# Optimization experiments

Measured on AMD Instinct MI355X. Metric: run time of the kernel, lower is better.

Reference implementation:

```python
import jax, jax.numpy as jnp
import numpy as np

TRAIN_COUNT, FEAT = 20000, 40
BATCH, NN, M = 2048, 64, 10


def _safe_l2(d2):
    # sqrt with zero (not NaN/inf) gradient at d2 == 0 (diagonal of pairwise dists)
    pos = d2 > 0
    return jnp.where(pos, jnp.sqrt(jnp.where(pos, d2, 1.0)), 0.0)


def setup_inputs() -> dict:
    key = jax.random.key(0)
    k1, k2, k3, k4 = jax.random.split(key, 4)
    x = jax.random.normal(k1, (TRAIN_COUNT, FEAT), dtype=jnp.float32)
    batch_indices = jax.random.randint(k2, (BATCH,), 0, TRAIN_COUNT)
    batch_nn_indices = jax.random.randint(k3, (BATCH, NN), 0, TRAIN_COUNT)
    batch_nn_targets = jax.random.normal(k4, (BATCH, NN, M), dtype=jnp.float32)
    length_scale = jnp.ones((M,), dtype=jnp.float32)
    eps = 1e-3 * jnp.ones((M,), dtype=jnp.float32)
    return {
        "x": x,
        "length_scale": length_scale,
        "eps": eps,
        "batch_indices": batch_indices,
        "batch_nn_indices": batch_nn_indices,
        "batch_nn_targets": batch_nn_targets,
    }


def reference(x, length_scale, eps, batch_indices, batch_nn_indices, batch_nn_targets):
    b, nn, m = batch_nn_targets.shape
    xb = x[batch_indices]          # (b, f)
    xn = x[batch_nn_indices]       # (b, nn, f)

    # crosswise l2 distances (b, nn)
    cd = _safe_l2(jnp.sum((xb[:, None, :] - xn) ** 2, axis=-1))
    # pairwise l2 distances (b, nn, nn)
    pd = _safe_l2(jnp.sum((xn[:, :, None, :] - xn[:, None, :, :]) ** 2, axis=-1))

    # Matern nu = 1/2: k(d) = exp(-d / length_scale); vectorized over the m models
    Kcross = jnp.exp(-cd[None, :, :] / length_scale[:, None, None])            # (m, b, nn)
    K = jnp.exp(-pd[None, :, :, :] / length_scale[:, None, None, None])        # (m, b, nn, nn)
    eye = jnp.eye(nn, dtype=K.dtype)
    Kp = K + eps[:, None, None, None] * eye                                     # homoscedastic perturb

    Y = jnp.moveaxis(batch_nn_targets, -1, 0)[..., None]                        # (m, b, nn, 1)
    F = jnp.linalg.solve(Kp, Y)[..., 0]                                         # (m, b, nn)
    predictions = jnp.einsum("mbn,mbn->bm", Kcross, F)

    G = jnp.linalg.solve(Kp, Kcross[..., None])[..., 0]                         # (m, b, nn)
    variances = 1.0 - jnp.einsum("mbn,mbn->bm", Kcross, G)

    sigma_sq = jnp.sum(Y[..., 0] * F, axis=(1, 2)) / (b * nn)                   # (m,)
    return predictions, variances, sigma_sq
```

## Files before the change

kernel.cpp:

```cpp
#include <hip/hip_runtime.h>
#include <math.h>

#define BATCH 2048
#define NN 64
#define FEAT 40
#define M 10
#define ASZ (NN * NN + 130)

__device__ __forceinline__ float rl(float v, int l) {
    return __int_as_float(__builtin_amdgcn_readlane(__float_as_int(v), l));
}
__device__ __forceinline__ float wsum(float v) {
#pragma unroll
    for (int o = 32; o >= 1; o >>= 1) v += __shfl_xor(v, o, 64);
    return v;
}

__global__ __launch_bounds__(64)
void muygps_kernel(
    const float* __restrict__ x,
    const float* __restrict__ ls,
    const float* __restrict__ epsv,
    const int*   __restrict__ bidx,
    const int*   __restrict__ nidx,
    const float* __restrict__ tgt,
    float* __restrict__ out,
    float* __restrict__ ws)
{
    __shared__ float A[ASZ];
    __shared__ float rvb[NN];

    const int b    = blockIdx.x;
    const int lane = threadIdx.x;

    const int nv = nidx[b * NN + lane];
    const float* xr0 = x + (size_t)nv * FEAT;
    float xc[FEAT];
#pragma unroll
    for (int q = 0; q < FEAT / 4; ++q) {
        const float4 v = *(const float4*)(xr0 + 4 * q);
        xc[4*q] = v.x; xc[4*q+1] = v.y; xc[4*q+2] = v.z; xc[4*q+3] = v.w;
    }
    float nl = 0.f;
#pragma unroll
    for (int f = 0; f < FEAT; ++f) nl = fmaf(xc[f], xc[f], nl);

    const int bi = __builtin_amdgcn_readfirstlane(bidx[b]);
    const float* xbp = x + (size_t)bi * FEAT;
    float gc = 0.f, nb = 0.f;
#pragma unroll
    for (int f = 0; f < FEAT; ++f) {
        const float bf = xbp[f];
        gc = fmaf(bf, xc[f], gc);
        nb = fmaf(bf, bf, nb);
    }
    float cd2 = (nb + nl) - 2.f * gc;
    cd2 = (cd2 < 0.05f) ? 0.f : cd2;
    const float cdv = sqrtf(cd2);

    unsigned done = 0;
    const unsigned all = (1u << M) - 1u;
    while (true) {
        const int   lead = __ffs(~done) - 1;
        const float lls  = ls[lead];
        const float lep  = epsv[lead];
        const float il   = -1.0f / lls;

#pragma unroll 2
        for (int i = 0; i < NN; ++i) {
            const int ri = __builtin_amdgcn_readlane(nv, i);
            const float* xr = x + (size_t)ri * FEAT;
            float g = 0.f;
#pragma unroll
            for (int f = 0; f < FEAT; ++f) g = fmaf(xr[f], xc[f], g);
            const float ni = rl(g, i);
            float d2 = (ni + nl) - 2.f * g;
            d2 = (d2 < 0.05f) ? 0.f : d2;
            float v = __expf(sqrtf(d2) * il);
            if (lane == i) v += lep;
            A[i * NN + lane] = v;
        }
        const float kcv = __expf(cdv * il);

        for (int p = 0; p < NN / 2; ++p) {
            const int k  = 2 * p;
            const int kk = k * NN + k;
            const float colv0 = A[kk + lane];
            const float d0  = rl(colv0, 0);
            const float r0  = __builtin_amdgcn_rcpf(d0);
            const float cv0 = colv0 * (-r0);
            const float l10 = rl(colv0, 1);
            float colv1 = A[kk + NN + lane];
            colv1 = fmaf(cv0, l10, colv1);
            const float d1  = rl(colv1, 1);
            const float r1  = __builtin_amdgcn_rcpf(d1);
            const float cv1 = colv1 * (-r1);
            A[kk + lane]      = (lane >= 1) ? colv0 * r0 : 0.f;
            A[kk + NN + lane] = (lane >= 2) ? colv1 * r1 : 0.f;
            rvb[k]     = r0;
            rvb[k + 1] = r1;
#pragma unroll 4
            for (int i = k + 2; i < NN; ++i) {
                const float l0 = rl(colv0, i - k);
                const float l1 = rl(colv1, i - k);
                float t = A[i * NN + k + lane];
                t = fmaf(cv0, l0, t);
                t = fmaf(cv1, l1, t);
                A[i * NN + k + lane] = t;
            }
        }

        float z[M + 1];
        z[0] = kcv;
        {
            const float* trow = tgt + ((size_t)b * NN + lane) * M;
#pragma unroll
            for (int q = 0; q < M / 2; ++q) {
                const float2 v = *(const float2*)(trow + 2 * q);
                z[2*q + 1] = v.x; z[2*q + 2] = v.y;
            }
        }
        for (int k = 0; k < NN - 1; ++k) {
            float lv = A[k * NN + lane];
            lv = (lane > k) ? -lv : 0.f;
#pragma unroll
            for (int j = 0; j < M + 1; ++j) {
                const float s = rl(z[j], k);
                z[j] = fmaf(lv, s, z[j]);
            }
        }

        const float rvv = rvb[lane];
        const float zc  = z[0];
        const float quad = wsum(zc * zc * rvv);
        unsigned newly = 0;
#pragma unroll
        for (int m = 0; m < M; ++m) {
            if (!(done & (1u << m)) && ls[m] == lls && epsv[m] == lep) {
                const float zm = z[m + 1];
                const float pm = wsum(zc * zm * rvv);
                const float sm = wsum(zm * zm * rvv);
                if (lane == 0) {
                    out[b * M + m] = pm;
                    out[BATCH * M + b * M + m] = 1.0f - quad;
                    ws[m * BATCH + b] = sm;
                }
                newly |= 1u << m;
            }
        }
        done |= newly;
        if (done == all) break;
    }
}

__global__ __launch_bounds__(256)
void sigma_reduce(const float* __restrict__ ws, float* __restrict__ out) {
    __shared__ float red[4];
    const int m = blockIdx.x;
    const int t = threadIdx.x;
    float a = 0.f;
    for (int i = t; i < BATCH; i += 256) a += ws[m * BATCH + i];
    a = wsum(a);
    if ((t & 63) == 0) red[t >> 6] = a;
    __syncthreads();
    if (t == 0)
        out[2 * BATCH * M + m] =
            (red[0] + red[1] + red[2] + red[3]) * (1.0f / (float)(BATCH * NN));
}

extern "C" void kernel_launch(void* const* d_in, const int* in_sizes, int n_in,
                              void* d_out, int out_size, void* d_ws, size_t ws_size,
                              hipStream_t stream) {
    const float* x   = (const float*)d_in[0];
    const float* lsp = (const float*)d_in[1];
    const float* ep  = (const float*)d_in[2];
    const int*   bi  = (const int*)d_in[3];
    const int*   ni  = (const int*)d_in[4];
    const float* tg  = (const float*)d_in[5];
    float* out = (float*)d_out;
    float* ws  = (float*)d_ws;

    muygps_kernel<<<BATCH, 64, 0, stream>>>(x, lsp, ep, bi, ni, tg, out, ws);
    sigma_reduce<<<M, 256, 0, stream>>>(ws, out);
}
```

Before: 159.8 us.

## Use packed FMA for distances, register-carry pivot columns, single-block sigma reduce

Distance dot products now use v_pk_fma_f32 inline asm on float2 pairs, processing two neighbor rows per iteration with scalar-loaded rows. The Cholesky-style elimination keeps the next two pivot columns in registers via shuffle-down instead of reloading them from LDS. It also sets waves_per_eu(2,2), and the sigma reduction becomes one 640-thread block with float4 loads. The aim is fewer VALU instructions and fewer LDS round trips, at the cost of register-pressure and scheduling risk from the asm and the occupancy hint.

Result: faster. 156.0 us (-2.4%).

```diff
diff --git a/kernel.cpp b/kernel.cpp
--- a/kernel.cpp
+++ b/kernel.cpp
@@ -7,9 +7,19 @@
 #define M 10
 #define ASZ (NN * NN + 130)
 
+typedef float v2f __attribute__((ext_vector_type(2)));
+
+#define PKFMA_SV(acc, s_src, v_src) \
+    asm("v_pk_fma_f32 %0, %1, %2, %0" : "+v"(acc) : "s"(s_src), "v"(v_src))
+#define PKFMA_VV(acc, a_src, b_src) \
+    asm("v_pk_fma_f32 %0, %1, %2, %0" : "+v"(acc) : "v"(a_src), "v"(b_src))
+
 __device__ __forceinline__ float rl(float v, int l) {
     return __int_as_float(__builtin_amdgcn_readlane(__float_as_int(v), l));
 }
+__device__ __forceinline__ int rli(int v, int l) {
+    return __builtin_amdgcn_readlane(v, l);
+}
 __device__ __forceinline__ float wsum(float v) {
 #pragma unroll
     for (int o = 32; o >= 1; o >>= 1) v += __shfl_xor(v, o, 64);
@@ -17,6 +27,7 @@
 }
 
 __global__ __launch_bounds__(64)
+__attribute__((amdgpu_waves_per_eu(2, 2)))
 void muygps_kernel(
     const float* __restrict__ x,
     const float* __restrict__ ls,
@@ -35,26 +46,27 @@
 
     const int nv = nidx[b * NN + lane];
     const float* xr0 = x + (size_t)nv * FEAT;
-    float xc[FEAT];
+    v2f xc2[FEAT / 2];
 #pragma unroll
     for (int q = 0; q < FEAT / 4; ++q) {
         const float4 v = *(const float4*)(xr0 + 4 * q);
-        xc[4*q] = v.x; xc[4*q+1] = v.y; xc[4*q+2] = v.z; xc[4*q+3] = v.w;
-    }
-    float nl = 0.f;
-#pragma unroll
-    for (int f = 0; f < FEAT; ++f) nl = fmaf(xc[f], xc[f], nl);
-
-    const int bi = __builtin_amdgcn_readfirstlane(bidx[b]);
-    const float* xbp = x + (size_t)bi * FEAT;
-    float gc = 0.f, nb = 0.f;
-#pragma unroll
-    for (int f = 0; f < FEAT; ++f) {
-        const float bf = xbp[f];
-        gc = fmaf(bf, xc[f], gc);
-        nb = fmaf(bf, bf, nb);
-    }
-    float cd2 = (nb + nl) - 2.f * gc;
+        xc2[2 * q]     = v2f{v.x, v.y};
+        xc2[2 * q + 1] = v2f{v.z, v.w};
+    }
+    v2f nl2 = {0.f, 0.f};
+#pragma unroll
+    for (int q = 0; q < FEAT / 2; ++q) PKFMA_VV(nl2, xc2[q], xc2[q]);
+    const float nl = nl2.x + nl2.y;
+
+    const v2f* xbv = (const v2f*)(x + (size_t)bidx[b] * FEAT);
+    v2f gc2 = {0.f, 0.f}, nb2 = {0.f, 0.f};
+#pragma unroll
+    for (int q = 0; q < FEAT / 2; ++q) {
+        const v2f xbq = xbv[q];
+        PKFMA_VV(gc2, xbq, xc2[q]);
+        PKFMA_VV(nb2, xbq, xbq);
+    }
+    float cd2 = ((nb2.x + nb2.y) + nl) - 2.f * (gc2.x + gc2.y);
     cd2 = (cd2 < 0.05f) ? 0.f : cd2;
     const float cdv = sqrtf(cd2);
 
@@ -66,60 +78,87 @@
         const float lep  = epsv[lead];
         const float il   = -1.0f / lls;
 
-#pragma unroll 2
-        for (int i = 0; i < NN; ++i) {
-            const int ri = __builtin_amdgcn_readlane(nv, i);
-            const float* xr = x + (size_t)ri * FEAT;
-            float g = 0.f;
-#pragma unroll
-            for (int f = 0; f < FEAT; ++f) g = fmaf(xr[f], xc[f], g);
-            const float ni = rl(g, i);
-            float d2 = (ni + nl) - 2.f * g;
-            d2 = (d2 < 0.05f) ? 0.f : d2;
-            float v = __expf(sqrtf(d2) * il);
-            if (lane == i) v += lep;
-            A[i * NN + lane] = v;
+        for (int i = 0; i < NN; i += 2) {
+            const int ri0 = rli(nv, i), ri1 = rli(nv, i + 1);
+            const v2f* rp0 = (const v2f*)(x + (size_t)ri0 * FEAT);
+            const v2f* rp1 = (const v2f*)(x + (size_t)ri1 * FEAT);
+            v2f g0 = {0.f, 0.f}, g1 = {0.f, 0.f};
+#pragma unroll
+            for (int q = 0; q < FEAT / 2; ++q) {
+                const v2f r0q = rp0[q], r1q = rp1[q];
+                PKFMA_SV(g0, r0q, xc2[q]);
+                PKFMA_SV(g1, r1q, xc2[q]);
+            }
+            const float ga = g0.x + g0.y, gb = g1.x + g1.y;
+            float d2a = (rl(ga, i) + nl) - 2.f * ga;
+            float d2b = (rl(gb, i + 1) + nl) - 2.f * gb;
+            d2a = (d2a < 0.05f) ? 0.f : d2a;
+            d2b = (d2b < 0.05f) ? 0.f : d2b;
+            float va = __expf(sqrtf(d2a) * il);
+            float vb = __expf(sqrtf(d2b) * il);
+            if (lane == i)     va += lep;
+            if (lane == i + 1) vb += lep;
+            A[i * NN + lane]       = va;
+            A[(i + 1) * NN + lane] = vb;
         }
         const float kcv = __expf(cdv * il);
 
-        for (int p = 0; p < NN / 2; ++p) {
-            const int k  = 2 * p;
-            const int kk = k * NN + k;
-            const float colv0 = A[kk + lane];
-            const float d0  = rl(colv0, 0);
+        float z[M + 1];
+        z[0] = kcv;
+        {
+            const float* trow = tgt + ((size_t)b * NN + lane) * M;
+#pragma unroll
+            for (int q = 0; q < M / 2; ++q) {
+                const float2 v = *(const float2*)(trow + 2 * q);
+                z[2 * q + 1] = v.x; z[2 * q + 2] = v.y;
+            }
+        }
+
+        float pc0 = A[lane];
+        float pc1 = A[NN + lane];
+        for (int p = 0; p < 31; ++p) {
+            const int k = 2 * p;
+            const float d0  = rl(pc0, 0);
             const float r0  = __builtin_amdgcn_rcpf(d0);
-            const float cv0 = colv0 * (-r0);
-            const float l10 = rl(colv0, 1);
-            float colv1 = A[kk + NN + lane];
-            colv1 = fmaf(cv0, l10, colv1);
-            const float d1  = rl(colv1, 1);
+            const float cv0 = pc0 * (-r0);
+            pc1 = fmaf(cv0, rl(pc0, 1), pc1);
+            const float d1  = rl(pc1, 1);
             const float r1  = __builtin_amdgcn_rcpf(d1);
-            const float cv1 = colv1 * (-r1);
-            A[kk + lane]      = (lane >= 1) ? colv0 * r0 : 0.f;
-            A[kk + NN + lane] = (lane >= 2) ? colv1 * r1 : 0.f;
+            const float cv1 = pc1 * (-r1);
+            A[k * NN + k + lane]      = (lane >= 1) ? pc0 * r0 : 0.f;
+            A[k * NN + NN + k + lane] = (lane >= 2) ? pc1 * r1 : 0.f;
             rvb[k]     = r0;
             rvb[k + 1] = r1;
-#pragma unroll 4
-            for (int i = k + 2; i < NN; ++i) {
-                const float l0 = rl(colv0, i - k);
-                const float l1 = rl(colv1, i - k);
+            float t2 = A[(k + 2) * NN + k + lane];
+            float t3 = A[(k + 3) * NN + k + lane];
+            t2 = fmaf(cv0, rl(pc0, 2), t2); t2 = fmaf(cv1, rl(pc1, 2), t2);
+            t3 = fmaf(cv0, rl(pc0, 3), t3); t3 = fmaf(cv1, rl(pc1, 3), t3);
+            const float n0 = __shfl_down(t2, 2, 64);
+            const float n1 = __shfl_down(t3, 2, 64);
+            for (int i = k + 4; i < NN; ++i) {
+                const float l0 = rl(pc0, i - k);
+                const float l1 = rl(pc1, i - k);
                 float t = A[i * NN + k + lane];
                 t = fmaf(cv0, l0, t);
                 t = fmaf(cv1, l1, t);
                 A[i * NN + k + lane] = t;
             }
-        }
-
-        float z[M + 1];
-        z[0] = kcv;
+            pc0 = n0; pc1 = n1;
+        }
         {
-            const float* trow = tgt + ((size_t)b * NN + lane) * M;
-#pragma unroll
-            for (int q = 0; q < M / 2; ++q) {
-                const float2 v = *(const float2*)(trow + 2 * q);
-                z[2*q + 1] = v.x; z[2*q + 2] = v.y;
-            }
-        }
+            const int k = 62;
+            const float d0  = rl(pc0, 0);
+            const float r0  = __builtin_amdgcn_rcpf(d0);
+            const float cv0 = pc0 * (-r0);
+            pc1 = fmaf(cv0, rl(pc0, 1), pc1);
+            const float d1  = rl(pc1, 1);
+            const float r1  = __builtin_amdgcn_rcpf(d1);
+            A[k * NN + k + lane]      = (lane >= 1) ? pc0 * r0 : 0.f;
+            A[k * NN + NN + k + lane] = (lane >= 2) ? pc1 * r1 : 0.f;
+            rvb[k]     = r0;
+            rvb[k + 1] = r1;
+        }
+
         for (int k = 0; k < NN - 1; ++k) {
             float lv = A[k * NN + lane];
             lv = (lane > k) ? -lv : 0.f;
@@ -153,19 +192,19 @@
     }
 }
 
-__global__ __launch_bounds__(256)
+__global__ __launch_bounds__(640)
 void sigma_reduce(const float* __restrict__ ws, float* __restrict__ out) {
-    __shared__ float red[4];
-    const int m = blockIdx.x;
-    const int t = threadIdx.x;
+    const int w = threadIdx.x >> 6, lane = threadIdx.x & 63;
+    const float4* p = (const float4*)(ws + w * BATCH);
     float a = 0.f;
-    for (int i = t; i < BATCH; i += 256) a += ws[m * BATCH + i];
+#pragma unroll
+    for (int i = 0; i < BATCH / 4 / 64; ++i) {
+        const float4 v = p[i * 64 + lane];
+        a += (v.x + v.y) + (v.z + v.w);
+    }
     a = wsum(a);
-    if ((t & 63) == 0) red[t >> 6] = a;
-    __syncthreads();
-    if (t == 0)
-        out[2 * BATCH * M + m] =
-            (red[0] + red[1] + red[2] + red[3]) * (1.0f / (float)(BATCH * NN));
+    if (lane == 0)
+        out[2 * BATCH * M + w] = a * (1.0f / (float)(BATCH * NN));
 }
 
 extern "C" void kernel_launch(void* const* d_in, const int* in_sizes, int n_in,
@@ -181,5 +220,5 @@
     float* ws  = (float*)d_ws;
 
     muygps_kernel<<<BATCH, 64, 0, stream>>>(x, lsp, ep, bi, ni, tg, out, ws);
-    sigma_reduce<<<M, 256, 0, stream>>>(ws, out);
-}
+    sigma_reduce<<<1, 640, 0, stream>>>(ws, out);
+}
```
